# Performance work log

Measured on AMD Instinct MI355X. Metric: run time of the kernel, lower is better.

The kernel has to match this reference:

```python
import jax, jax.numpy as jnp
import numpy as np

N = 50000      # graph nodes
E = 800000     # edges
R = 8          # relations
D = 128        # entity_dim == relation_dim == n_hidden
L = 2          # gnn layers
NE = 150000    # entity vocab
NEG_SLOPE = 0.01


def setup_inputs() -> dict:
    key = jax.random.key(0)
    ks = jax.random.split(key, 9)
    return {
        "node_ids": jax.random.randint(ks[0], (N,), 0, NE),
        "relation_ids": jax.random.randint(ks[1], (E,), 0, R),
        "src": jax.random.randint(ks[2], (E,), 0, N),
        "dst": jax.random.randint(ks[3], (E,), 0, N),
        "entity_table": jax.random.normal(ks[4], (NE, D), dtype=jnp.float32) * 0.1,
        "relation_table": jax.random.normal(ks[5], (R, D), dtype=jnp.float32) * 0.1,
        "relation_W": jax.random.normal(ks[6], (R, D, D), dtype=jnp.float32) * 0.1,
        "res_fc_W": jax.random.normal(ks[7], (L, D, D), dtype=jnp.float32) * 0.1,
        "res_fc2_W": jax.random.normal(ks[8], (L, D, D), dtype=jnp.float32) * 0.1,
    }


def _kgat_layer(h, efeat, rel, src, dst, relation_W, W1, W2):
    # project every node by every relation weight: (N, R, D)
    proj = jnp.einsum('nd,rde->nre', h, relation_W)
    t_r = proj[src, rel]            # (E, D)  W_r h_src
    h_r = proj[dst, rel]            # (E, D)  W_r h_dst
    # att = (W_r h_t)^T tanh(W_r h_dst + e_r)
    att = jnp.sum(t_r * jnp.tanh(h_r + efeat), axis=1)  # (E,)
    # edge softmax over incoming edges of each dst node
    m = jax.ops.segment_max(att, dst, num_segments=N)
    ex = jnp.exp(att - m[dst])
    s = jax.ops.segment_sum(ex, dst, num_segments=N)
    a = ex / s[dst]                 # (E,)
    # message = a * h_src, scatter-sum to dst
    h_nb = jax.ops.segment_sum(h[src] * a[:, None], dst, num_segments=N)  # (N, D)
    out = (jax.nn.leaky_relu((h + h_nb) @ W1.T, NEG_SLOPE)
           + jax.nn.leaky_relu((h * h_nb) @ W2.T, NEG_SLOPE))
    return h_nb, out


def reference(node_ids, relation_ids, src, dst, entity_table, relation_table,
              relation_W, res_fc_W, res_fc2_W):
    h = entity_table[node_ids]           # (N, D)
    efeat = relation_table[relation_ids]  # (E, D)
    cache = [h]
    for i in range(L):
        h, out = _kgat_layer(h, efeat, relation_ids, src, dst,
                             relation_W, res_fc_W[i], res_fc2_W[i])
        cache.append(out)
    return jnp.concatenate(cache, axis=1)  # (N, D*(L+1))
```

## Files before the change

kernel.cpp:

```cpp
#include <hip/hip_runtime.h>
#include <math.h>

#define DDIM 128
#define RREL 8

typedef __attribute__((ext_vector_type(8))) short bf16x8;
typedef __attribute__((ext_vector_type(4))) float f32x4;

static __device__ __forceinline__ float bf2f(unsigned short h) {
    union { unsigned u; float f; } c; c.u = ((unsigned)h) << 16; return c.f;
}
static __device__ __forceinline__ unsigned short f2bf(float f) {
    union { float f; unsigned u; } c; c.f = f;
    unsigned r = (c.u + 0x7FFFu + ((c.u >> 16) & 1u)) >> 16;
    return (unsigned short)r;
}
static __device__ __forceinline__ float lrelu(float x) {
    return x > 0.0f ? x : 0.01f * x;
}

__global__ __launch_bounds__(256) void prep_weights(const float* __restrict__ relW,
                                                    const float* __restrict__ fcW,
                                                    const float* __restrict__ fc2W,
                                                    unsigned short* __restrict__ Wt,
                                                    unsigned short* __restrict__ Wb1,
                                                    unsigned short* __restrict__ Wb2) {
    int i = blockIdx.x * 256 + threadIdx.x;
    const int NT = RREL * DDIM * DDIM;
    const int NF = 2 * DDIM * DDIM;
    if (i < NT) {
        int r = i >> 14;
        int d = (i >> 7) & 127;
        int e = i & 127;
        Wt[(r << 14) + (e << 7) + d] = f2bf(relW[i]);
    } else if (i < NT + NF) {
        int j = i - NT;
        Wb1[j] = f2bf(fcW[j]);
    } else if (i < NT + 2 * NF) {
        int j = i - NT - NF;
        Wb2[j] = f2bf(fc2W[j]);
    }
}

__global__ __launch_bounds__(256) void gather_h0(const int* __restrict__ node_ids,
                                                 const float* __restrict__ etab,
                                                 unsigned short* __restrict__ hb0,
                                                 float* __restrict__ out, int N) {
    int i = blockIdx.x * 256 + threadIdx.x;
    if (i >= N * 32) return;
    int n = i >> 5;
    int c4 = (i & 31) * 4;
    float4 v = *(const float4*)(etab + (size_t)node_ids[n] * DDIM + c4);
    *(float4*)(out + (size_t)n * 384 + c4) = v;
    *(ushort4*)(hb0 + (size_t)n * DDIM + c4) =
        make_ushort4(f2bf(v.x), f2bf(v.y), f2bf(v.z), f2bf(v.w));
}

__global__ __launch_bounds__(256) void hist_k(const int* __restrict__ dst,
                                              int* __restrict__ counts, int E) {
    int i = blockIdx.x * 256 + threadIdx.x;
    if (i < E) atomicAdd(counts + dst[i], 1);
}

__global__ __launch_bounds__(256) void scan_a(const int* __restrict__ counts,
                                              int* __restrict__ tmp,
                                              int* __restrict__ part, int N) {
    __shared__ int sh[256];
    int i = blockIdx.x * 256 + threadIdx.x;
    int v = (i < N) ? counts[i] : 0;
    sh[threadIdx.x] = v;
    __syncthreads();
    #pragma unroll
    for (int o = 1; o < 256; o <<= 1) {
        int t = (threadIdx.x >= o) ? sh[threadIdx.x - o] : 0;
        __syncthreads();
        sh[threadIdx.x] += t;
        __syncthreads();
    }
    if (i < N) tmp[i] = sh[threadIdx.x];
    if (threadIdx.x == 255) part[blockIdx.x] = sh[255];
}

__global__ __launch_bounds__(256) void scan_b(int* __restrict__ part, int nb) {
    __shared__ int sh[256];
    int v = (threadIdx.x < nb) ? part[threadIdx.x] : 0;
    sh[threadIdx.x] = v;
    __syncthreads();
    #pragma unroll
    for (int o = 1; o < 256; o <<= 1) {
        int t = (threadIdx.x >= o) ? sh[threadIdx.x - o] : 0;
        __syncthreads();
        sh[threadIdx.x] += t;
        __syncthreads();
    }
    if (threadIdx.x < nb) part[threadIdx.x] = sh[threadIdx.x] - v;
}

__global__ __launch_bounds__(256) void scan_c(const int* __restrict__ counts,
                                              const int* __restrict__ tmp,
                                              const int* __restrict__ part,
                                              int* __restrict__ row_ptr,
                                              int* __restrict__ woff, int N) {
    int i = blockIdx.x * 256 + threadIdx.x;
    if (i >= N) return;
    int incl = tmp[i] + part[blockIdx.x];
    row_ptr[i + 1] = incl;
    woff[i] = incl - counts[i];
    if (i == 0) row_ptr[0] = 0;
}

__global__ __launch_bounds__(256) void scatter_k(const int* __restrict__ src,
                                                 const int* __restrict__ rel,
                                                 const int* __restrict__ dst,
                                                 int* __restrict__ woff,
                                                 int2* __restrict__ epack, int E) {
    int i = blockIdx.x * 256 + threadIdx.x;
    if (i >= E) return;
    int p = atomicAdd(woff + dst[i], 1);
    epack[p] = make_int2(src[i], rel[i]);
}

__global__ __launch_bounds__(256) void proj_gemm(const unsigned short* __restrict__ hb,
                                                 const unsigned short* __restrict__ Wt,
                                                 unsigned short* __restrict__ proj, int N) {
    __shared__ __align__(16) unsigned short As[64][136];
    __shared__ __align__(16) unsigned short Bs[128][136];
    int tid = threadIdx.x;
    int row0 = blockIdx.x * 64;
    int wave = tid >> 6, lane = tid & 63;
    int m = lane & 15, quad = lane >> 4;

    #pragma unroll
    for (int j = 0; j < 4; ++j) {
        int idx = j * 256 + tid;
        int row = idx >> 4;
        int c8 = (idx & 15) * 8;
        int grow = row0 + row;
        uint4 v = make_uint4(0, 0, 0, 0);
        if (grow < N) v = *(const uint4*)(hb + (size_t)grow * DDIM + c8);
        *(uint4*)(&As[row][c8]) = v;
    }

    bf16x8 afrag[4];
    #pragma unroll
    for (int r = 0; r < RREL; ++r) {
        const unsigned short* B = Wt + ((size_t)r << 14);
        #pragma unroll
        for (int j = 0; j < 8; ++j) {
            int idx = j * 256 + tid;
            int brow = idx >> 4;
            int c8 = (idx & 15) * 8;
            *(uint4*)(&Bs[brow][c8]) = *(const uint4*)(B + ((size_t)brow << 7) + c8);
        }
        __syncthreads();
        if (r == 0) {
            #pragma unroll
            for (int kk = 0; kk < 4; ++kk)
                afrag[kk] = *(const bf16x8*)(&As[wave * 16 + m][kk * 32 + quad * 8]);
        }
        f32x4 acc[8];
        #pragma unroll
        for (int t = 0; t < 8; ++t) acc[t] = (f32x4){0.f, 0.f, 0.f, 0.f};
        #pragma unroll
        for (int kk = 0; kk < 4; ++kk) {
            #pragma unroll
            for (int t = 0; t < 8; ++t) {
                bf16x8 b = *(const bf16x8*)(&Bs[t * 16 + m][kk * 32 + quad * 8]);
                acc[t] = __builtin_amdgcn_mfma_f32_16x16x32_bf16(afrag[kk], b, acc[t], 0, 0, 0);
            }
        }
        #pragma unroll
        for (int t = 0; t < 8; ++t) {
            #pragma unroll
            for (int q = 0; q < 4; ++q) {
                int row = row0 + wave * 16 + quad * 4 + q;
                if (row < N)
                    proj[((size_t)row * RREL + r) * DDIM + t * 16 + m] = f2bf(acc[t][q]);
            }
        }
        __syncthreads();
    }
}

__global__ __launch_bounds__(256) void fused_agg(const unsigned short* __restrict__ proj,
                                                 const unsigned short* __restrict__ hb,
                                                 const float* __restrict__ rtab,
                                                 const int* __restrict__ row_ptr,
                                                 const int2* __restrict__ epack,
                                                 float* __restrict__ hnb,
                                                 unsigned short* __restrict__ hbn, int N) {
    __shared__ float th[4][RREL][DDIM];
    int wv = threadIdx.x >> 6, lane = threadIdx.x & 63;
    int n = blockIdx.x * 4 + wv;
    if (n >= N) return;
    int d0 = lane * 2;

    #pragma unroll
    for (int r = 0; r < RREL; ++r) {
        unsigned pv = *(const unsigned*)(proj + ((size_t)n * RREL + r) * DDIM + d0);
        float2 rv = *(const float2*)(rtab + r * DDIM + d0);
        th[wv][r][d0]     = tanhf(bf2f(pv & 0xffff) + rv.x);
        th[wv][r][d0 + 1] = tanhf(bf2f(pv >> 16) + rv.y);
    }

    int beg = row_ptr[n], end = row_ptr[n + 1];
    float m = -INFINITY, s = 0.f, a0 = 0.f, a1 = 0.f;

    for (int base = beg; base < end; base += 64) {
        int cnt = min(64, end - base);
        int2 ep = make_int2(0, 0);
        if (base + lane < end) ep = epack[base + lane];
        for (int j = 0; j < cnt; ++j) {
            int sr = __shfl(ep.x, j, 64);
            int rr = __shfl(ep.y, j, 64);
            unsigned tv = *(const unsigned*)(proj + ((size_t)sr * RREL + rr) * DDIM + d0);
            unsigned hv = *(const unsigned*)(hb + (size_t)sr * DDIM + d0);
            float2 t2 = *(const float2*)(&th[wv][rr][d0]);
            float v = bf2f(tv & 0xffff) * t2.x + bf2f(tv >> 16) * t2.y;
            #pragma unroll
            for (int o = 32; o > 0; o >>= 1) v += __shfl_xor(v, o, 64);
            float mn = fmaxf(m, v);
            float sc = __expf(m - mn);
            float p  = __expf(v - mn);
            s = s * sc + p;
            a0 = a0 * sc + p * bf2f(hv & 0xffff);
            a1 = a1 * sc + p * bf2f(hv >> 16);
            m = mn;
        }
    }
    float inv = (end > beg) ? 1.0f / s : 0.0f;
    a0 *= inv; a1 *= inv;
    hnb[(size_t)n * DDIM + d0]     = a0;
    hnb[(size_t)n * DDIM + d0 + 1] = a1;
    *(unsigned*)(hbn + (size_t)n * DDIM + d0) =
        (unsigned)f2bf(a0) | ((unsigned)f2bf(a1) << 16);
}

__global__ __launch_bounds__(256) void out_gemm(const unsigned short* __restrict__ hb,
                                                const float* __restrict__ hnb,
                                                const unsigned short* __restrict__ W1,
                                                const unsigned short* __restrict__ W2,
                                                float* __restrict__ out,
                                                int colbase, int N) {
    __shared__ __align__(16) unsigned short As[64][136];
    __shared__ __align__(16) unsigned short Bs[128][136];
    int tid = threadIdx.x;
    int row0 = blockIdx.x * 64;
    int wave = tid >> 6, lane = tid & 63;
    int m = lane & 15, quad = lane >> 4;

    f32x4 acc[2][8];
    #pragma unroll
    for (int p = 0; p < 2; ++p)
        #pragma unroll
        for (int t = 0; t < 8; ++t) acc[p][t] = (f32x4){0.f, 0.f, 0.f, 0.f};

    #pragma unroll
    for (int p = 0; p < 2; ++p) {
        #pragma unroll
        for (int j = 0; j < 4; ++j) {
            int idx = j * 256 + tid;
            int row = idx >> 4;
            int c8 = (idx & 15) * 8;
            int grow = row0 + row;
            unsigned pk[4] = {0, 0, 0, 0};
            if (grow < N) {
                uint4 hv = *(const uint4*)(hb + (size_t)grow * DDIM + c8);
                const float* np = hnb + (size_t)grow * DDIM + c8;
                float4 n0 = *(const float4*)np;
                float4 n1 = *(const float4*)(np + 4);
                float hf[8] = {bf2f(hv.x & 0xffff), bf2f(hv.x >> 16),
                               bf2f(hv.y & 0xffff), bf2f(hv.y >> 16),
                               bf2f(hv.z & 0xffff), bf2f(hv.z >> 16),
                               bf2f(hv.w & 0xffff), bf2f(hv.w >> 16)};
                float nf[8] = {n0.x, n0.y, n0.z, n0.w, n1.x, n1.y, n1.z, n1.w};
                #pragma unroll
                for (int jj = 0; jj < 4; ++jj) {
                    float v0 = p ? hf[2 * jj] * nf[2 * jj] : hf[2 * jj] + nf[2 * jj];
                    float v1 = p ? hf[2 * jj + 1] * nf[2 * jj + 1] : hf[2 * jj + 1] + nf[2 * jj + 1];
                    pk[jj] = (unsigned)f2bf(v0) | ((unsigned)f2bf(v1) << 16);
                }
            }
            *(uint4*)(&As[row][c8]) = make_uint4(pk[0], pk[1], pk[2], pk[3]);
        }
        const unsigned short* W = p ? W2 : W1;
        #pragma unroll
        for (int j = 0; j < 8; ++j) {
            int idx = j * 256 + tid;
            int brow = idx >> 4;
            int c8 = (idx & 15) * 8;
            *(uint4*)(&Bs[brow][c8]) = *(const uint4*)(W + ((size_t)brow << 7) + c8);
        }
        __syncthreads();

        #pragma unroll
        for (int kk = 0; kk < 4; ++kk) {
            bf16x8 a = *(const bf16x8*)(&As[wave * 16 + m][kk * 32 + quad * 8]);
            #pragma unroll
            for (int t = 0; t < 8; ++t) {
                bf16x8 b = *(const bf16x8*)(&Bs[t * 16 + m][kk * 32 + quad * 8]);
                acc[p][t] = __builtin_amdgcn_mfma_f32_16x16x32_bf16(a, b, acc[p][t], 0, 0, 0);
            }
        }
        __syncthreads();
    }

    #pragma unroll
    for (int t = 0; t < 8; ++t) {
        #pragma unroll
        for (int q = 0; q < 4; ++q) {
            int row = row0 + wave * 16 + quad * 4 + q;
            int col = t * 16 + m;
            if (row < N)
                out[(size_t)row * 384 + colbase + col] =
                    lrelu(acc[0][t][q]) + lrelu(acc[1][t][q]);
        }
    }
}

extern "C" void kernel_launch(void* const* d_in, const int* in_sizes, int n_in,
                              void* d_out, int out_size, void* d_ws, size_t ws_size,
                              hipStream_t stream) {
    const int* node_ids = (const int*)d_in[0];
    const int* rel_ids  = (const int*)d_in[1];
    const int* src      = (const int*)d_in[2];
    const int* dst      = (const int*)d_in[3];
    const float* etab   = (const float*)d_in[4];
    const float* rtab   = (const float*)d_in[5];
    const float* relW   = (const float*)d_in[6];
    const float* fcW    = (const float*)d_in[7];
    const float* fc2W   = (const float*)d_in[8];
    float* out = (float*)d_out;

    const int N = in_sizes[0];
    const int E = in_sizes[1];
    const int NB = (N + 255) / 256;

    char* ws = (char*)d_ws;
    size_t off = 0;
    auto alloc = [&](size_t bytes) -> char* {
        char* p = ws + off;
        off = (off + bytes + 255) & ~(size_t)255;
        return p;
    };
    unsigned short* hb[3];
    hb[0] = (unsigned short*)alloc((size_t)N * DDIM * 2);
    hb[1] = (unsigned short*)alloc((size_t)N * DDIM * 2);
    hb[2] = (unsigned short*)alloc((size_t)N * DDIM * 2);
    float* hnb = (float*)alloc((size_t)N * DDIM * 4);
    unsigned short* Wt  = (unsigned short*)alloc((size_t)RREL * DDIM * DDIM * 2);
    unsigned short* Wb1 = (unsigned short*)alloc((size_t)2 * DDIM * DDIM * 2);
    unsigned short* Wb2 = (unsigned short*)alloc((size_t)2 * DDIM * DDIM * 2);
    unsigned short* proj = (unsigned short*)alloc((size_t)N * RREL * DDIM * 2);
    int*  counts  = (int*)alloc((size_t)N * 4);
    int*  tmp     = (int*)alloc((size_t)N * 4);
    int*  part    = (int*)alloc((size_t)NB * 4);
    int*  row_ptr = (int*)alloc((size_t)(N + 1) * 4);
    int*  woff    = (int*)alloc((size_t)N * 4);
    int2* epack   = (int2*)alloc((size_t)E * 8);

    const int NW = RREL * DDIM * DDIM + 4 * DDIM * DDIM;
    hipLaunchKernelGGL(prep_weights, dim3((NW + 255) / 256), dim3(256), 0, stream,
                       relW, fcW, fc2W, Wt, Wb1, Wb2);
    hipLaunchKernelGGL(gather_h0, dim3((N * 32 + 255) / 256), dim3(256), 0, stream,
                       node_ids, etab, hb[0], out, N);

    hipMemsetAsync(counts, 0, (size_t)N * 4, stream);
    hipLaunchKernelGGL(hist_k, dim3((E + 255) / 256), dim3(256), 0, stream, dst, counts, E);
    hipLaunchKernelGGL(scan_a, dim3(NB), dim3(256), 0, stream, counts, tmp, part, N);
    hipLaunchKernelGGL(scan_b, dim3(1), dim3(256), 0, stream, part, NB);
    hipLaunchKernelGGL(scan_c, dim3(NB), dim3(256), 0, stream, counts, tmp, part, row_ptr, woff, N);
    hipLaunchKernelGGL(scatter_k, dim3((E + 255) / 256), dim3(256), 0, stream,
                       src, rel_ids, dst, woff, epack, E);

    for (int l = 0; l < 2; ++l) {
        hipLaunchKernelGGL(proj_gemm, dim3((N + 63) / 64), dim3(256), 0, stream,
                           hb[l], Wt, proj, N);
        hipLaunchKernelGGL(fused_agg, dim3((N + 3) / 4), dim3(256), 0, stream,
                           proj, hb[l], rtab, row_ptr, epack, hnb, hb[l + 1], N);
        hipLaunchKernelGGL(out_gemm, dim3((N + 63) / 64), dim3(256), 0, stream,
                           hb[l], hnb, Wb1 + (size_t)l * DDIM * DDIM, Wb2 + (size_t)l * DDIM * DDIM,
                           out, (l + 1) * DDIM, N);
    }
}
```

Baseline: 588.4 us.

## Process eight edges per wave in aggregation with split online softmax merge

The aggregation kernel now splits each wave into eight groups of eight lanes. Each group handles one edge at a time with 16 features per lane and 16-byte loads, and keeps its own online-softmax state; the groups' states are merged with cross-lane shuffles at the end. This replaces the serial one-edge-per-wave loop with its full 64-lane reduction per edge. The change also swaps tanhf for an exp-based tanh and drops the fp32 h_nb buffer, so out_gemm reads the bf16 copy instead. The cost is more registers per lane and slightly lower precision for h_nb in the output GEMM.

```diff
diff --git a/kernel.cpp b/kernel.cpp
--- a/kernel.cpp
+++ b/kernel.cpp
@@ -9,6 +9,12 @@
 
 static __device__ __forceinline__ float bf2f(unsigned short h) {
     union { unsigned u; float f; } c; c.u = ((unsigned)h) << 16; return c.f;
+}
+static __device__ __forceinline__ float bf2f_lo(unsigned w) {
+    union { unsigned u; float f; } c; c.u = w << 16; return c.f;
+}
+static __device__ __forceinline__ float bf2f_hi(unsigned w) {
+    union { unsigned u; float f; } c; c.u = w & 0xffff0000u; return c.f;
 }
 static __device__ __forceinline__ unsigned short f2bf(float f) {
     union { float f; unsigned u; } c; c.f = f;
@@ -18,6 +24,11 @@
 static __device__ __forceinline__ float lrelu(float x) {
     return x > 0.0f ? x : 0.01f * x;
 }
+static __device__ __forceinline__ float tanh_fast(float x) {
+    return 1.0f - 2.0f / (__expf(2.0f * x) + 1.0f);
+}
+
+#define NEGSENT -3.0e38f
 
 __global__ __launch_bounds__(256) void prep_weights(const float* __restrict__ relW,
                                                     const float* __restrict__ fcW,
@@ -187,57 +198,121 @@
                                                  const float* __restrict__ rtab,
                                                  const int* __restrict__ row_ptr,
                                                  const int2* __restrict__ epack,
-                                                 float* __restrict__ hnb,
                                                  unsigned short* __restrict__ hbn, int N) {
     __shared__ float th[4][RREL][DDIM];
     int wv = threadIdx.x >> 6, lane = threadIdx.x & 63;
     int n = blockIdx.x * 4 + wv;
     if (n >= N) return;
+    int g  = lane >> 3;
+    int gp = lane & 7;
     int d0 = lane * 2;
+    int dbase = gp * 16;
 
     #pragma unroll
     for (int r = 0; r < RREL; ++r) {
         unsigned pv = *(const unsigned*)(proj + ((size_t)n * RREL + r) * DDIM + d0);
         float2 rv = *(const float2*)(rtab + r * DDIM + d0);
-        th[wv][r][d0]     = tanhf(bf2f(pv & 0xffff) + rv.x);
-        th[wv][r][d0 + 1] = tanhf(bf2f(pv >> 16) + rv.y);
+        th[wv][r][d0]     = tanh_fast(bf2f_lo(pv) + rv.x);
+        th[wv][r][d0 + 1] = tanh_fast(bf2f_hi(pv) + rv.y);
     }
 
     int beg = row_ptr[n], end = row_ptr[n + 1];
-    float m = -INFINITY, s = 0.f, a0 = 0.f, a1 = 0.f;
-
-    for (int base = beg; base < end; base += 64) {
-        int cnt = min(64, end - base);
-        int2 ep = make_int2(0, 0);
-        if (base + lane < end) ep = epack[base + lane];
-        for (int j = 0; j < cnt; ++j) {
-            int sr = __shfl(ep.x, j, 64);
-            int rr = __shfl(ep.y, j, 64);
-            unsigned tv = *(const unsigned*)(proj + ((size_t)sr * RREL + rr) * DDIM + d0);
-            unsigned hv = *(const unsigned*)(hb + (size_t)sr * DDIM + d0);
-            float2 t2 = *(const float2*)(&th[wv][rr][d0]);
-            float v = bf2f(tv & 0xffff) * t2.x + bf2f(tv >> 16) * t2.y;
-            #pragma unroll
-            for (int o = 32; o > 0; o >>= 1) v += __shfl_xor(v, o, 64);
-            float mn = fmaxf(m, v);
-            float sc = __expf(m - mn);
-            float p  = __expf(v - mn);
-            s = s * sc + p;
-            a0 = a0 * sc + p * bf2f(hv & 0xffff);
-            a1 = a1 * sc + p * bf2f(hv >> 16);
-            m = mn;
-        }
-    }
+    float m = NEGSENT, s = 0.f;
+    float a[16];
+    #pragma unroll
+    for (int i = 0; i < 16; ++i) a[i] = 0.f;
+
+    for (int base = beg; base < end; base += 8) {
+        int eidx = base + g;
+        bool act = eidx < end;
+        int2 ep = act ? epack[eidx] : make_int2(0, 0);
+        int sr = ep.x, rr = ep.y;
+        const unsigned short* pp = proj + ((size_t)sr * RREL + rr) * DDIM + dbase;
+        const unsigned short* hp = hb + (size_t)sr * DDIM + dbase;
+        uint4 pv0 = *(const uint4*)(pp);
+        uint4 pv1 = *(const uint4*)(pp + 8);
+        uint4 hv0 = *(const uint4*)(hp);
+        uint4 hv1 = *(const uint4*)(hp + 8);
+        const float* tp = &th[wv][rr][dbase];
+        float4 t0 = *(const float4*)(tp);
+        float4 t1 = *(const float4*)(tp + 4);
+        float4 t2 = *(const float4*)(tp + 8);
+        float4 t3 = *(const float4*)(tp + 12);
+
+        float v;
+        {
+            unsigned pw0 = pv0.x, pw1 = pv0.y, pw2 = pv0.z, pw3 = pv0.w;
+            unsigned pw4 = pv1.x, pw5 = pv1.y, pw6 = pv1.z, pw7 = pv1.w;
+            v  = bf2f_lo(pw0) * t0.x + bf2f_hi(pw0) * t0.y;
+            v += bf2f_lo(pw1) * t0.z + bf2f_hi(pw1) * t0.w;
+            v += bf2f_lo(pw2) * t1.x + bf2f_hi(pw2) * t1.y;
+            v += bf2f_lo(pw3) * t1.z + bf2f_hi(pw3) * t1.w;
+            v += bf2f_lo(pw4) * t2.x + bf2f_hi(pw4) * t2.y;
+            v += bf2f_lo(pw5) * t2.z + bf2f_hi(pw5) * t2.w;
+            v += bf2f_lo(pw6) * t3.x + bf2f_hi(pw6) * t3.y;
+            v += bf2f_lo(pw7) * t3.z + bf2f_hi(pw7) * t3.w;
+        }
+        v += __shfl_xor(v, 1, 64);
+        v += __shfl_xor(v, 2, 64);
+        v += __shfl_xor(v, 4, 64);
+        if (!act) v = NEGSENT;
+
+        float mn = fmaxf(m, v);
+        float sc = __expf(m - mn);
+        float p  = act ? __expf(v - mn) : 0.f;
+        s = s * sc + p;
+        float h0 = p * bf2f_lo(hv0.x), h1 = p * bf2f_hi(hv0.x);
+        float h2 = p * bf2f_lo(hv0.y), h3 = p * bf2f_hi(hv0.y);
+        float h4 = p * bf2f_lo(hv0.z), h5 = p * bf2f_hi(hv0.z);
+        float h6 = p * bf2f_lo(hv0.w), h7 = p * bf2f_hi(hv0.w);
+        a[0] = a[0] * sc + h0;  a[1] = a[1] * sc + h1;
+        a[2] = a[2] * sc + h2;  a[3] = a[3] * sc + h3;
+        a[4] = a[4] * sc + h4;  a[5] = a[5] * sc + h5;
+        a[6] = a[6] * sc + h6;  a[7] = a[7] * sc + h7;
+        float h8 = p * bf2f_lo(hv1.x), h9  = p * bf2f_hi(hv1.x);
+        float ha = p * bf2f_lo(hv1.y), hb_ = p * bf2f_hi(hv1.y);
+        float hc = p * bf2f_lo(hv1.z), hd  = p * bf2f_hi(hv1.z);
+        float he = p * bf2f_lo(hv1.w), hf  = p * bf2f_hi(hv1.w);
+        a[8]  = a[8]  * sc + h8;  a[9]  = a[9]  * sc + h9;
+        a[10] = a[10] * sc + ha;  a[11] = a[11] * sc + hb_;
+        a[12] = a[12] * sc + hc;  a[13] = a[13] * sc + hd;
+        a[14] = a[14] * sc + he;  a[15] = a[15] * sc + hf;
+        m = mn;
+    }
+
+    #pragma unroll
+    for (int st = 8; st < 64; st <<= 1) {
+        float m2 = __shfl_xor(m, st, 64);
+        float s2 = __shfl_xor(s, st, 64);
+        float mn = fmaxf(m, m2);
+        float sc1 = __expf(m - mn);
+        float sc2 = __expf(m2 - mn);
+        s = s * sc1 + s2 * sc2;
+        #pragma unroll
+        for (int i = 0; i < 16; ++i) {
+            float a2 = __shfl_xor(a[i], st, 64);
+            a[i] = a[i] * sc1 + a2 * sc2;
+        }
+        m = mn;
+    }
+
     float inv = (end > beg) ? 1.0f / s : 0.0f;
-    a0 *= inv; a1 *= inv;
-    hnb[(size_t)n * DDIM + d0]     = a0;
-    hnb[(size_t)n * DDIM + d0 + 1] = a1;
-    *(unsigned*)(hbn + (size_t)n * DDIM + d0) =
-        (unsigned)f2bf(a0) | ((unsigned)f2bf(a1) << 16);
+    #pragma unroll
+    for (int i = 0; i < 16; ++i) a[i] *= inv;
+
+    if (g == 0) {
+        unsigned short* bp = hbn + (size_t)n * DDIM + gp * 16;
+        unsigned pk[8];
+        #pragma unroll
+        for (int i = 0; i < 8; ++i)
+            pk[i] = (unsigned)f2bf(a[2 * i]) | ((unsigned)f2bf(a[2 * i + 1]) << 16);
+        *(uint4*)(bp)     = make_uint4(pk[0], pk[1], pk[2], pk[3]);
+        *(uint4*)(bp + 8) = make_uint4(pk[4], pk[5], pk[6], pk[7]);
+    }
 }
 
 __global__ __launch_bounds__(256) void out_gemm(const unsigned short* __restrict__ hb,
-                                                const float* __restrict__ hnb,
+                                                const unsigned short* __restrict__ hbn,
                                                 const unsigned short* __restrict__ W1,
                                                 const unsigned short* __restrict__ W2,
                                                 float* __restrict__ out,
@@ -266,18 +341,15 @@
             unsigned pk[4] = {0, 0, 0, 0};
             if (grow < N) {
                 uint4 hv = *(const uint4*)(hb + (size_t)grow * DDIM + c8);
-                const float* np = hnb + (size_t)grow * DDIM + c8;
-                float4 n0 = *(const float4*)np;
-                float4 n1 = *(const float4*)(np + 4);
-                float hf[8] = {bf2f(hv.x & 0xffff), bf2f(hv.x >> 16),
-                               bf2f(hv.y & 0xffff), bf2f(hv.y >> 16),
-                               bf2f(hv.z & 0xffff), bf2f(hv.z >> 16),
-                               bf2f(hv.w & 0xffff), bf2f(hv.w >> 16)};
-                float nf[8] = {n0.x, n0.y, n0.z, n0.w, n1.x, n1.y, n1.z, n1.w};
+                uint4 nv = *(const uint4*)(hbn + (size_t)grow * DDIM + c8);
+                unsigned hw[4] = {hv.x, hv.y, hv.z, hv.w};
+                unsigned nw[4] = {nv.x, nv.y, nv.z, nv.w};
                 #pragma unroll
                 for (int jj = 0; jj < 4; ++jj) {
-                    float v0 = p ? hf[2 * jj] * nf[2 * jj] : hf[2 * jj] + nf[2 * jj];
-                    float v1 = p ? hf[2 * jj + 1] * nf[2 * jj + 1] : hf[2 * jj + 1] + nf[2 * jj + 1];
+                    float hlo = bf2f_lo(hw[jj]), hhi = bf2f_hi(hw[jj]);
+                    float nlo = bf2f_lo(nw[jj]), nhi = bf2f_hi(nw[jj]);
+                    float v0 = p ? hlo * nlo : hlo + nlo;
+                    float v1 = p ? hhi * nhi : hhi + nhi;
                     pk[jj] = (unsigned)f2bf(v0) | ((unsigned)f2bf(v1) << 16);
                 }
             }
@@ -347,7 +419,6 @@
     hb[0] = (unsigned short*)alloc((size_t)N * DDIM * 2);
     hb[1] = (unsigned short*)alloc((size_t)N * DDIM * 2);
     hb[2] = (unsigned short*)alloc((size_t)N * DDIM * 2);
-    float* hnb = (float*)alloc((size_t)N * DDIM * 4);
     unsigned short* Wt  = (unsigned short*)alloc((size_t)RREL * DDIM * DDIM * 2);
     unsigned short* Wb1 = (unsigned short*)alloc((size_t)2 * DDIM * DDIM * 2);
     unsigned short* Wb2 = (unsigned short*)alloc((size_t)2 * DDIM * DDIM * 2);
@@ -377,9 +448,9 @@
         hipLaunchKernelGGL(proj_gemm, dim3((N + 63) / 64), dim3(256), 0, stream,
                            hb[l], Wt, proj, N);
         hipLaunchKernelGGL(fused_agg, dim3((N + 3) / 4), dim3(256), 0, stream,
-                           proj, hb[l], rtab, row_ptr, epack, hnb, hb[l + 1], N);
+                           proj, hb[l], rtab, row_ptr, epack, hb[l + 1], N);
         hipLaunchKernelGGL(out_gemm, dim3((N + 63) / 64), dim3(256), 0, stream,
-                           hb[l], hnb, Wb1 + (size_t)l * DDIM * DDIM, Wb2 + (size_t)l * DDIM * DDIM,
+                           hb[l], hb[l + 1], Wb1 + (size_t)l * DDIM * DDIM, Wb2 + (size_t)l * DDIM * DDIM,
                            out, (l + 1) * DDIM, N);
     }
 }
```

New measurement: 515.3 us. -12.4%, faster.
